# Kernel tuning notes

Measured on AMD Instinct MI355X. Metric: run time of the kernel, lower is better.

## Reference

```python
import jax, jax.numpy as jnp
import numpy as np

B, S, E = 2, 1024, 1024
H, DH = 16, 64           # num_heads, key_dim = E // H
MAXLEN = 2048            # config.max_sequence_length -> table size 2*MAXLEN-1


def setup_inputs() -> dict:
    key = jax.random.key(0)
    ks = jax.random.split(key, 13)
    sc = 1.0 / np.sqrt(E)
    return {
        "query": jax.random.normal(ks[0], (B, S, E), jnp.float32),
        "key": jax.random.normal(ks[1], (B, S, E), jnp.float32),
        "value": jax.random.normal(ks[2], (B, S, E), jnp.float32),
        "Wq": jax.random.normal(ks[3], (E, E), jnp.float32) * sc,
        "bq": jnp.zeros((E,), jnp.float32),
        "Wk": jax.random.normal(ks[4], (E, E), jnp.float32) * sc,
        "bk": jnp.zeros((E,), jnp.float32),
        "Wv": jax.random.normal(ks[5], (E, E), jnp.float32) * sc,
        "bv": jnp.zeros((E,), jnp.float32),
        "Wo": jax.random.normal(ks[6], (E, E), jnp.float32) * sc,
        "bo": jnp.zeros((E,), jnp.float32),
        "rel_pos_emb": jax.random.normal(ks[7], (2 * MAXLEN - 1, DH), jnp.float32) * 0.02,
        "rel_pos_bias": jnp.zeros((2 * MAXLEN - 1,), jnp.float32),
    }


def _split_heads(x):
    # [B, S, E] -> [B, H, S, DH]
    return x.reshape(B, S, H, DH).transpose(0, 2, 1, 3)


def _relative_shift(x):
    # x: [B, H, S, S]; pad one zero column on the left of the last dim,
    # reshape to [B, H, S+1, S], drop the first row -> [B, H, S, S]
    x = jnp.pad(x, ((0, 0), (0, 0), (0, 0), (1, 0)))
    x = x.reshape(B, H, S + 1, S)
    return x[:, :, 1:, :]


def reference(query, key, value, Wq, bq, Wk, bk, Wv, bv, Wo, bo,
              rel_pos_emb, rel_pos_bias):
    q = _split_heads(query @ Wq + bq) / jnp.sqrt(jnp.float32(DH))  # [B,H,S,DH]
    k = _split_heads(key @ Wk + bk)                                 # [B,H,S,DH]
    v = _split_heads(value @ Wv + bv)                               # [B,H,S,DH]

    scores = jnp.einsum("bhid,bhjd->bhij", q, k)  # [B,H,S,S]

    # relative position term (gather + skew, as in the original call())
    pos_ids = jnp.arange(S)[:, None] - jnp.arange(S)[None, :] + (MAXLEN - 1)  # [S,S]
    rpe = rel_pos_emb[pos_ids]    # [S, S, DH]
    rpb = rel_pos_bias[pos_ids]   # [S, S]
    rel = jnp.einsum("bhid,ijd->bhij", q, rpe)  # [B,H,S,S]
    rel = _relative_shift(rel)
    scores = scores + rel + rpb   # rpb broadcasts over [B,H]

    weights = jax.nn.softmax(scores, axis=-1)
    out = jnp.einsum("bhij,bhjd->bhid", weights, v)  # [B,H,S,DH]
    out = out.transpose(0, 2, 1, 3).reshape(B, S, E)
    return out @ Wo + bo
```

## Files before the change

### kernel.cpp

```cpp
#include <hip/hip_runtime.h>

typedef unsigned short u16;
typedef __bf16 bf16_t;
typedef bf16_t bf16x8 __attribute__((ext_vector_type(8)));
typedef u16 u16x8 __attribute__((ext_vector_type(8)));
typedef float f32x4 __attribute__((ext_vector_type(4)));

#define DEVI __device__ __forceinline__


DEVI u16 f2bf(float f) {
    unsigned u = __builtin_bit_cast(unsigned, f);
    u = (u + 0x7FFFu + ((u >> 16) & 1u)) >> 16;
    return (u16)u;
}
DEVI float bf2f(u16 b) {
    unsigned u = ((unsigned)b) << 16;
    return __builtin_bit_cast(float, u);
}
DEVI f32x4 mfma16(u16x8 a, u16x8 b, f32x4 c) {
    return __builtin_amdgcn_mfma_f32_16x16x32_bf16(
        __builtin_bit_cast(bf16x8, a), __builtin_bit_cast(bf16x8, b), c, 0, 0, 0);
}
DEVI void gl2lds(const u16* g, u16* l) {
    __builtin_amdgcn_global_load_lds(
        (__attribute__((address_space(1))) void*)g,
        (__attribute__((address_space(3))) void*)l, 16, 0, 0);
}

__global__ __launch_bounds__(256) void cvt_kernel(
    const float* __restrict__ q, const float* __restrict__ k, const float* __restrict__ v,
    const float* __restrict__ emb,
    u16* __restrict__ xq, u16* __restrict__ xk, u16* __restrict__ xv, u16* __restrict__ embb)
{
    const long NQ = 2097152;
    const long NE = 262080;
    long i4 = ((long)blockIdx.x * 256 + threadIdx.x) * 4;
    if (i4 < 3 * NQ) {
        int which = (int)(i4 >> 21);
        long off = i4 & (NQ - 1);
        const float* src = which == 0 ? q : (which == 1 ? k : v);
        u16* dst = which == 0 ? xq : (which == 1 ? xk : xv);
        float4 f = *(const float4*)(src + off);
        ushort4 o; o.x = f2bf(f.x); o.y = f2bf(f.y); o.z = f2bf(f.z); o.w = f2bf(f.w);
        *(ushort4*)(dst + off) = o;
    } else {
        long off = i4 - 3 * NQ;
        if (off < NE) {
            float4 f = *(const float4*)(emb + off);
            ushort4 o; o.x = f2bf(f.x); o.y = f2bf(f.y); o.z = f2bf(f.z); o.w = f2bf(f.w);
            *(ushort4*)(embb + off) = o;
        }
    }
}

__global__ __launch_bounds__(256) void wt_kernel(
    const float* __restrict__ w0, const float* __restrict__ w1,
    const float* __restrict__ w2, const float* __restrict__ w3,
    u16* __restrict__ t0, u16* __restrict__ t1, u16* __restrict__ t2, u16* __restrict__ t3)
{
    int z = blockIdx.z;
    const float* W = z == 0 ? w0 : (z == 1 ? w1 : (z == 2 ? w2 : w3));
    u16* T = z == 0 ? t0 : (z == 1 ? t1 : (z == 2 ? t2 : t3));
    __shared__ float tile[64][65];
    int k0 = blockIdx.y * 64, n0 = blockIdx.x * 64;
    int tx = threadIdx.x, ty = threadIdx.y;
    for (int r = ty; r < 64; r += 4)
        tile[r][tx] = W[(long)(k0 + r) * 1024 + n0 + tx];
    __syncthreads();
    for (int r = ty; r < 64; r += 4)
        T[(long)(n0 + r) * 1024 + k0 + tx] = f2bf(tile[tx][r]);
}

template<int MT>
__global__ __launch_bounds__(256) void gemm_kernel(
    const u16* __restrict__ A0, const u16* __restrict__ A1, const u16* __restrict__ A2,
    const u16* __restrict__ W0, const u16* __restrict__ W1, const u16* __restrict__ W2,
    const float* __restrict__ bias0, const float* __restrict__ bias1, const float* __restrict__ bias2,
    u16* __restrict__ o0, u16* __restrict__ o1, u16* __restrict__ o2,
    float* __restrict__ ofp, int mode_base)
{
    int z = blockIdx.z;
    int mode = mode_base + z;
    const u16* A = z == 0 ? A0 : (z == 1 ? A1 : A2);
    const u16* W = z == 0 ? W0 : (z == 1 ? W1 : W2);
    const float* bias = z == 0 ? bias0 : (z == 1 ? bias1 : bias2);
    u16* ob = z == 0 ? o0 : (z == 1 ? o1 : o2);

    constexpr int MROWS = MT * 32;
    __shared__ u16 la[2 * MROWS * 32];
    __shared__ u16 lw[2 * 128 * 32];

    int lin = blockIdx.x + (blockIdx.y << 3);
    int xcd = lin & 7, idx = lin >> 3;
    int xt = (xcd & 1) * 4 + (idx & 3);
    int yt = (xcd >> 1) * 8 + (idx >> 2);
    int m0 = yt * MROWS, n0 = xt * 128;

    int t = threadIdx.x, lane = t & 63, wid = t >> 6;
    int l15 = lane & 15, quad = lane >> 4;
    int wm = (wid >> 1) * (MT * 16), wn = (wid & 1) * 64;
    int sr = lane >> 2, sp = lane & 3;

    f32x4 acc[MT][4] = {};

    auto stage = [&](int buf, int k0) {
#pragma unroll
        for (int q = 0; q < MT / 2; q++) {
            int r = wid * (MT * 8) + q * 16 + sr;
            int c = sp ^ ((r >> 1) & 3);
            gl2lds(A + (long)(m0 + r) * 1024 + k0 + c * 8,
                   la + buf * (MROWS * 32) + (wid * (MT * 8) + q * 16) * 32);
        }
#pragma unroll
        for (int q = 0; q < 2; q++) {
            int r = wid * 32 + q * 16 + sr;
            int c = sp ^ ((r >> 1) & 3);
            gl2lds(W + (long)(n0 + r) * 1024 + k0 + c * 8,
                   lw + buf * (128 * 32) + (wid * 32 + q * 16) * 32);
        }
    };

    stage(0, 0);
    __syncthreads();
    int cur = 0;
#pragma unroll 1
    for (int k0 = 0; k0 < 1024; k0 += 32) {
        if (k0 < 992) stage(cur ^ 1, k0 + 32);
        const u16* lab = la + cur * (MROWS * 32);
        const u16* lwb = lw + cur * (128 * 32);
        u16x8 af[MT], bfr[4];
#pragma unroll
        for (int mt = 0; mt < MT; mt++) {
            int r = wm + mt * 16 + l15;
            af[mt] = *(const u16x8*)&lab[r * 32 + ((quad ^ ((r >> 1) & 3)) * 8)];
        }
#pragma unroll
        for (int nt = 0; nt < 4; nt++) {
            int r = wn + nt * 16 + l15;
            bfr[nt] = *(const u16x8*)&lwb[r * 32 + ((quad ^ ((r >> 1) & 3)) * 8)];
        }
#pragma unroll
        for (int mt = 0; mt < MT; mt++)
#pragma unroll
            for (int nt = 0; nt < 4; nt++)
                acc[mt][nt] = mfma16(af[mt], bfr[nt], acc[mt][nt]);
        __syncthreads();
        cur ^= 1;
    }

#pragma unroll
    for (int mt = 0; mt < MT; mt++)
#pragma unroll
        for (int nt = 0; nt < 4; nt++)
#pragma unroll
            for (int reg = 0; reg < 4; reg++) {
                int gm = m0 + wm + mt * 16 + quad * 4 + reg;
                int gn = n0 + wn + nt * 16 + l15;
                float val = acc[mt][nt][reg] + bias[gn];
                if (mode == 0) {
                    val *= 0.125f;
                    long o = ((long)((gm >> 10) * 16 + (gn >> 6)) << 16) + ((gm & 1023) << 6) + (gn & 63);
                    ob[o] = f2bf(val);
                } else if (mode == 1) {
                    long o = ((long)((gm >> 10) * 16 + (gn >> 6)) << 16) + ((gm & 1023) << 6) + (gn & 63);
                    ob[o] = f2bf(val);
                } else if (mode == 2) {
                    long o = ((long)((gm >> 10) * 16 + (gn >> 6)) << 16) + ((long)(gn & 63) << 10) + (gm & 1023);
                    ob[o] = f2bf(val);
                } else {
                    ofp[(long)gm * 1024 + gn] = val;
                }
            }
}

__global__ __launch_bounds__(256) void gc_kernel(
    const u16* __restrict__ qb, const u16* __restrict__ embb,
    const float* __restrict__ rpb, u16* __restrict__ Bskew)
{
    int u0 = blockIdx.x * 32;
    int i0 = u0 & 1023;
    int t = threadIdx.x, lane = t & 63, wid = t >> 6;
    int l15 = lane & 15, quad = lane >> 4;

    __shared__ float lds_rpb[2048];
    for (int j = t; j < 1024; j += 256) {
        lds_rpb[j] = rpb[j + 2047];
        lds_rpb[1024 + j] = rpb[j + 1022];
    }
    __syncthreads();

    u16x8 aq[2][2];
#pragma unroll
    for (int rg = 0; rg < 2; rg++) {
        long qoff = (long)(u0 + rg * 16 + l15) * 64 + quad * 8;
        aq[rg][0] = *(const u16x8*)&qb[qoff];
        aq[rg][1] = *(const u16x8*)&qb[qoff + 32];
    }

    u16x8 nb0, nb1;
    {
        long ebase = (long)(1024 + i0 + wid * 16 + l15) * 64 + quad * 8;
        nb0 = *(const u16x8*)&embb[ebase];
        nb1 = *(const u16x8*)&embb[ebase + 32];
    }

    for (int tt = wid; tt < 66; tt += 4) {
        u16x8 b0 = nb0, b1 = nb1;
        if (tt + 4 < 66) {
            long ebase = (long)(1024 + i0 + (tt + 4) * 16 + l15) * 64 + quad * 8;
            nb0 = *(const u16x8*)&embb[ebase];
            nb1 = *(const u16x8*)&embb[ebase + 32];
        }
        int w0 = tt * 16;
#pragma unroll
        for (int rg = 0; rg < 2; rg++) {
            f32x4 c = {};
            c = mfma16(aq[rg][0], b0, c);
            c = mfma16(aq[rg][1], b1, c);
#pragma unroll
            for (int reg = 0; reg < 4; reg++) {
                int row = rg * 16 + quad * 4 + reg;
                int cc = w0 + l15 - row;
                if ((unsigned)cc <= 1023u) {
                    int i = i0 + row;
                    float rb = lds_rpb[cc + ((cc <= i) ? 0 : 1024)];
                    Bskew[((long)(u0 + row) << 10) + cc] = f2bf(c[reg] + rb);
                }
            }
        }
    }
}

__global__ __launch_bounds__(256, 4) void flash_kernel(
    const u16* __restrict__ qb, const u16* __restrict__ kb, const u16* __restrict__ vT,
    const u16* __restrict__ Bskew, const float* __restrict__ rpb,
    float* __restrict__ Po, float* __restrict__ Pm, float* __restrict__ Pl)
{
    int itile = blockIdx.x;
    int bh = blockIdx.y;
    int js = blockIdx.z;
    int t = threadIdx.x, lane = t & 63, wid = t >> 6;
    int l15 = lane & 15, quad = lane >> 4;
    int i0w = itile * 64 + wid * 16;

    __shared__ u16 lds_k[64 * 64];
    __shared__ u16 lds_v[64 * 64];
    __shared__ u16 lds_p[4][16][72];

    int sr8 = lane >> 3, sp8 = lane & 7;

    float rpb2046 = rpb[2046];

    u16x8 aq[2];
    {
        long qoff = ((long)(bh * 1024) + i0w + l15) * 64 + quad * 8;
        aq[0] = *(const u16x8*)&qb[qoff];
        aq[1] = *(const u16x8*)&qb[qoff + 32];
    }
    float m_r[4], l_r[4];
    f32x4 o_acc[4] = {};
#pragma unroll
    for (int r = 0; r < 4; r++) { m_r[r] = -1e30f; l_r[r] = 0.f; }

    const u16* kbase = kb + (long)bh * 65536;
    const u16* vbase = vT + (long)bh * 65536;
    const u16* bbase = Bskew + ((long)bh << 20);

    for (int jt = 0; jt < 8; jt++) {
        int j0 = js * 512 + jt * 64;
        __syncthreads();
#pragma unroll
        for (int q = 0; q < 2; q++) {
            int r = wid * 16 + q * 8 + sr8;
            int c = sp8 ^ (r & 7);
            gl2lds(kbase + (long)(j0 + r) * 64 + c * 8, lds_k + (wid * 16 + q * 8) * 64);
            gl2lds(vbase + (long)r * 1024 + j0 + c * 8, lds_v + (wid * 16 + q * 8) * 64);
        }
        __syncthreads();

        f32x4 s_acc[4];
#pragma unroll
        for (int nt = 0; nt < 4; nt++) {
            int r = nt * 16 + l15;
            u16x8 b0 = *(const u16x8*)&lds_k[r * 64 + ((quad ^ (r & 7)) * 8)];
            u16x8 b1 = *(const u16x8*)&lds_k[r * 64 + (((quad + 4) ^ (r & 7)) * 8)];
            f32x4 c = {};
            c = mfma16(aq[0], b0, c);
            c = mfma16(aq[1], b1, c);
            s_acc[nt] = c;
        }

#pragma unroll
        for (int nt = 0; nt < 4; nt++) {
            int jn0 = j0 + nt * 16;
            int jj = jn0 + l15;
            if (jn0 + 15 <= i0w) {
#pragma unroll
                for (int reg = 0; reg < 4; reg++) {
                    int ii = i0w + quad * 4 + reg;
                    s_acc[nt][reg] += bf2f(bbase[((long)ii << 10) + (ii - jj)]);
                }
            } else if (jn0 >= i0w + 17) {
#pragma unroll
                for (int reg = 0; reg < 4; reg++) {
                    int ii = i0w + quad * 4 + reg;
                    s_acc[nt][reg] += bf2f(bbase[((long)(ii + 1) << 10) + (ii + 1025 - jj)]);
                }
            } else {
#pragma unroll
                for (int reg = 0; reg < 4; reg++) {
                    int ii = i0w + quad * 4 + reg;
                    float a;
                    if (jj <= ii)          a = bf2f(bbase[((long)ii << 10) + (ii - jj)]);
                    else if (jj == ii + 1) a = rpb2046;
                    else                   a = bf2f(bbase[((long)(ii + 1) << 10) + (ii + 1025 - jj)]);
                    s_acc[nt][reg] += a;
                }
            }
        }

#pragma unroll
        for (int reg = 0; reg < 4; reg++) {
            float mx = fmaxf(fmaxf(s_acc[0][reg], s_acc[1][reg]), fmaxf(s_acc[2][reg], s_acc[3][reg]));
            for (int off = 1; off < 16; off <<= 1) mx = fmaxf(mx, __shfl_xor(mx, off, 64));
            float mnew = fmaxf(m_r[reg], mx);
            float alpha = __expf(m_r[reg] - mnew);
            float rs = 0.f;
#pragma unroll
            for (int nt = 0; nt < 4; nt++) {
                float p = __expf(s_acc[nt][reg] - mnew);
                s_acc[nt][reg] = p;
                rs += p;
            }
            for (int off = 1; off < 16; off <<= 1) rs += __shfl_xor(rs, off, 64);
            l_r[reg] = l_r[reg] * alpha + rs;
            m_r[reg] = mnew;
#pragma unroll
            for (int dt = 0; dt < 4; dt++) o_acc[dt][reg] *= alpha;
        }

#pragma unroll
        for (int nt = 0; nt < 4; nt++)
#pragma unroll
            for (int reg = 0; reg < 4; reg++)
                lds_p[wid][quad * 4 + reg][nt * 16 + l15] = f2bf(s_acc[nt][reg]);

        u16x8 pf0 = *(const u16x8*)&lds_p[wid][l15][quad * 8];
        u16x8 pf1 = *(const u16x8*)&lds_p[wid][l15][quad * 8 + 32];
#pragma unroll
        for (int dt = 0; dt < 4; dt++) {
            int r = dt * 16 + l15;
            u16x8 v0 = *(const u16x8*)&lds_v[r * 64 + ((quad ^ (r & 7)) * 8)];
            u16x8 v1 = *(const u16x8*)&lds_v[r * 64 + (((quad + 4) ^ (r & 7)) * 8)];
            o_acc[dt] = mfma16(pf0, v0, o_acc[dt]);
            o_acc[dt] = mfma16(pf1, v1, o_acc[dt]);
        }
    }

    int blk = (js * 32 + bh) * 16 + itile;
    float* PoB = Po + (long)blk * 4096;
#pragma unroll
    for (int dt = 0; dt < 4; dt++)
#pragma unroll
        for (int reg = 0; reg < 4; reg++) {
            int rr = wid * 16 + quad * 4 + reg;
            PoB[rr * 64 + dt * 16 + l15] = o_acc[dt][reg];
        }
    if (l15 == 0) {
#pragma unroll
        for (int reg = 0; reg < 4; reg++) {
            int rr = wid * 16 + quad * 4 + reg;
            Pm[blk * 64 + rr] = m_r[reg];
            Pl[blk * 64 + rr] = l_r[reg];
        }
    }
}

__global__ __launch_bounds__(256) void combine_kernel(
    const float* __restrict__ Po, const float* __restrict__ Pm, const float* __restrict__ Pl,
    u16* __restrict__ attn)
{
    int itile = blockIdx.x, bh = blockIdx.y;
    int t = threadIdx.x;
    int c = t & 63, rg = t >> 6;
    int blk0 = bh * 16 + itile;
    int blk1 = (32 + bh) * 16 + itile;
    int b = bh >> 4, h = bh & 15;
    for (int rr = rg; rr < 64; rr += 4) {
        float m0 = Pm[blk0 * 64 + rr], m1 = Pm[blk1 * 64 + rr];
        float ms = fmaxf(m0, m1);
        float e0 = __expf(m0 - ms), e1 = __expf(m1 - ms);
        float l = Pl[blk0 * 64 + rr] * e0 + Pl[blk1 * 64 + rr] * e1;
        float o = Po[(long)blk0 * 4096 + rr * 64 + c] * e0
                + Po[(long)blk1 * 4096 + rr * 64 + c] * e1;
        int ii = itile * 64 + rr;
        attn[((long)(b * 1024 + ii)) * 1024 + h * 64 + c] = f2bf(o / l);
    }
}

extern "C" void kernel_launch(void* const* d_in, const int* in_sizes, int n_in,
                              void* d_out, int out_size, void* d_ws, size_t ws_size,
                              hipStream_t stream)
{
    const float* query = (const float*)d_in[0];
    const float* key_  = (const float*)d_in[1];
    const float* value = (const float*)d_in[2];
    const float* Wq = (const float*)d_in[3];
    const float* bq = (const float*)d_in[4];
    const float* Wk = (const float*)d_in[5];
    const float* bk = (const float*)d_in[6];
    const float* Wv = (const float*)d_in[7];
    const float* bv = (const float*)d_in[8];
    const float* Wo = (const float*)d_in[9];
    const float* bo = (const float*)d_in[10];
    const float* emb = (const float*)d_in[11];
    const float* rpb = (const float*)d_in[12];

    char* ws = (char*)d_ws;
    u16* xq   = (u16*)(ws + 0);
    u16* xk   = (u16*)(ws + 4194304);
    u16* xv   = (u16*)(ws + 8388608);
    u16* WqT  = (u16*)(ws + 12582912);
    u16* WkT  = (u16*)(ws + 14680064);
    u16* WvT  = (u16*)(ws + 16777216);
    u16* embb = (u16*)(ws + 18874368);
    u16* WoT  = (u16*)(ws + 19922944);
    u16* qb   = (u16*)(ws + 22020096);
    u16* kb   = (u16*)(ws + 26214400);
    u16* vT   = (u16*)(ws + 30408704);
    u16* Bskew= (u16*)(ws + 34603008);
    float* Po = (float*)(ws + 0);
    float* Pm = (float*)(ws + 16777216);
    float* Pl = (float*)(ws + 17039360);
    u16* attn = (u16*)(ws + 22020096);

    cvt_kernel<<<6400, 256, 0, stream>>>(query, key_, value, emb, xq, xk, xv, embb);
    wt_kernel<<<dim3(16, 16, 4), dim3(64, 4), 0, stream>>>(Wq, Wk, Wv, Wo, WqT, WkT, WvT, WoT);
    gemm_kernel<2><<<dim3(8, 32, 3), 256, 0, stream>>>(xq, xk, xv, WqT, WkT, WvT,
                                                       bq, bk, bv, qb, kb, vT, nullptr, 0);
    gc_kernel<<<1024, 256, 0, stream>>>(qb, embb, rpb, Bskew);
    flash_kernel<<<dim3(16, 32, 2), 256, 0, stream>>>(qb, kb, vT, Bskew, rpb, Po, Pm, Pl);
    combine_kernel<<<dim3(16, 32), 256, 0, stream>>>(Po, Pm, Pl, attn);
    gemm_kernel<2><<<dim3(8, 32, 1), 256, 0, stream>>>(attn, nullptr, nullptr, WoT, nullptr, nullptr,
                                                       bo, nullptr, nullptr,
                                                       nullptr, nullptr, nullptr, (float*)d_out, 3);
}
```

Measured before the change: 240.1 us.

## Double-buffer K/V tiles and prefetch skewed bias one iteration ahead

Switches the flash attention kernel to double-buffered LDS for the K and V tiles, so the next tile is issued while the current one is computed, and drops one barrier per iteration. It also prefetches the skewed relative-position bias values for the next tile into registers, taking scattered global-load latency off the critical path. In exchange, LDS use doubles and register pressure rises (16 extra prefetch registers), and occupancy is lowered from 4 to 3 blocks per SIMD in launch bounds. The diagonal tile's special case now loads a dummy element and overrides it with rpb[2046].

```diff
diff --git a/kernel.cpp b/kernel.cpp
--- a/kernel.cpp
+++ b/kernel.cpp
@@ -232,7 +232,7 @@
     }
 }
 
-__global__ __launch_bounds__(256, 4) void flash_kernel(
+__global__ __launch_bounds__(256, 3) void flash_kernel(
     const u16* __restrict__ qb, const u16* __restrict__ kb, const u16* __restrict__ vT,
     const u16* __restrict__ Bskew, const float* __restrict__ rpb,
     float* __restrict__ Po, float* __restrict__ Pm, float* __restrict__ Pl)
@@ -244,8 +244,8 @@
     int l15 = lane & 15, quad = lane >> 4;
     int i0w = itile * 64 + wid * 16;
 
-    __shared__ u16 lds_k[64 * 64];
-    __shared__ u16 lds_v[64 * 64];
+    __shared__ u16 lds_k[2][64 * 64];
+    __shared__ u16 lds_v[2][64 * 64];
     __shared__ u16 lds_p[4][16][72];
 
     int sr8 = lane >> 3, sp8 = lane & 7;
@@ -267,24 +267,64 @@
     const u16* vbase = vT + (long)bh * 65536;
     const u16* bbase = Bskew + ((long)bh << 20);
 
-    for (int jt = 0; jt < 8; jt++) {
-        int j0 = js * 512 + jt * 64;
-        __syncthreads();
+    auto stage = [&](int buf, int j0) {
 #pragma unroll
         for (int q = 0; q < 2; q++) {
             int r = wid * 16 + q * 8 + sr8;
             int c = sp8 ^ (r & 7);
-            gl2lds(kbase + (long)(j0 + r) * 64 + c * 8, lds_k + (wid * 16 + q * 8) * 64);
-            gl2lds(vbase + (long)r * 1024 + j0 + c * 8, lds_v + (wid * 16 + q * 8) * 64);
-        }
-        __syncthreads();
+            gl2lds(kbase + (long)(j0 + r) * 64 + c * 8, &lds_k[buf][(wid * 16 + q * 8) * 64]);
+            gl2lds(vbase + (long)r * 1024 + j0 + c * 8, &lds_v[buf][(wid * 16 + q * 8) * 64]);
+        }
+    };
+    auto ldb = [&](int j0, unsigned short* b) {
+#pragma unroll
+        for (int nt = 0; nt < 4; nt++) {
+            int jn0 = j0 + nt * 16;
+            int jj = jn0 + l15;
+            if (jn0 + 15 <= i0w) {
+#pragma unroll
+                for (int reg = 0; reg < 4; reg++) {
+                    int ii = i0w + quad * 4 + reg;
+                    b[nt * 4 + reg] = bbase[((long)ii << 10) + (ii - jj)];
+                }
+            } else if (jn0 >= i0w + 17) {
+#pragma unroll
+                for (int reg = 0; reg < 4; reg++) {
+                    int ii = i0w + quad * 4 + reg;
+                    b[nt * 4 + reg] = bbase[((long)(ii + 1) << 10) + (ii + 1025 - jj)];
+                }
+            } else {
+#pragma unroll
+                for (int reg = 0; reg < 4; reg++) {
+                    int ii = i0w + quad * 4 + reg;
+                    long off = (jj <= ii) ? (((long)ii << 10) + (ii - jj))
+                             : ((jj == ii + 1) ? ((long)ii << 10)
+                                               : (((long)(ii + 1) << 10) + (ii + 1025 - jj)));
+                    b[nt * 4 + reg] = bbase[off];
+                }
+            }
+        }
+    };
+
+    unsigned short bcur[16], bnxt[16];
+    stage(0, js * 512);
+    ldb(js * 512, bcur);
+    __syncthreads();
+
+    int cur = 0;
+    for (int jt = 0; jt < 8; jt++) {
+        int j0 = js * 512 + jt * 64;
+        if (jt < 7) {
+            stage(cur ^ 1, j0 + 64);
+            ldb(j0 + 64, bnxt);
+        }
 
         f32x4 s_acc[4];
 #pragma unroll
         for (int nt = 0; nt < 4; nt++) {
             int r = nt * 16 + l15;
-            u16x8 b0 = *(const u16x8*)&lds_k[r * 64 + ((quad ^ (r & 7)) * 8)];
-            u16x8 b1 = *(const u16x8*)&lds_k[r * 64 + (((quad + 4) ^ (r & 7)) * 8)];
+            u16x8 b0 = *(const u16x8*)&lds_k[cur][r * 64 + ((quad ^ (r & 7)) * 8)];
+            u16x8 b1 = *(const u16x8*)&lds_k[cur][r * 64 + (((quad + 4) ^ (r & 7)) * 8)];
             f32x4 c = {};
             c = mfma16(aq[0], b0, c);
             c = mfma16(aq[1], b1, c);
@@ -295,28 +335,13 @@
         for (int nt = 0; nt < 4; nt++) {
             int jn0 = j0 + nt * 16;
             int jj = jn0 + l15;
-            if (jn0 + 15 <= i0w) {
-#pragma unroll
-                for (int reg = 0; reg < 4; reg++) {
-                    int ii = i0w + quad * 4 + reg;
-                    s_acc[nt][reg] += bf2f(bbase[((long)ii << 10) + (ii - jj)]);
-                }
-            } else if (jn0 >= i0w + 17) {
-#pragma unroll
-                for (int reg = 0; reg < 4; reg++) {
-                    int ii = i0w + quad * 4 + reg;
-                    s_acc[nt][reg] += bf2f(bbase[((long)(ii + 1) << 10) + (ii + 1025 - jj)]);
-                }
-            } else {
-#pragma unroll
-                for (int reg = 0; reg < 4; reg++) {
-                    int ii = i0w + quad * 4 + reg;
-                    float a;
-                    if (jj <= ii)          a = bf2f(bbase[((long)ii << 10) + (ii - jj)]);
-                    else if (jj == ii + 1) a = rpb2046;
-                    else                   a = bf2f(bbase[((long)(ii + 1) << 10) + (ii + 1025 - jj)]);
-                    s_acc[nt][reg] += a;
-                }
+            bool mixed = (jn0 + 15 > i0w) && (jn0 < i0w + 17);
+#pragma unroll
+            for (int reg = 0; reg < 4; reg++) {
+                int ii = i0w + quad * 4 + reg;
+                float a = bf2f(bcur[nt * 4 + reg]);
+                if (mixed && jj == ii + 1) a = rpb2046;
+                s_acc[nt][reg] += a;
             }
         }
 
@@ -351,10 +376,17 @@
 #pragma unroll
         for (int dt = 0; dt < 4; dt++) {
             int r = dt * 16 + l15;
-            u16x8 v0 = *(const u16x8*)&lds_v[r * 64 + ((quad ^ (r & 7)) * 8)];
-            u16x8 v1 = *(const u16x8*)&lds_v[r * 64 + (((quad + 4) ^ (r & 7)) * 8)];
+            u16x8 v0 = *(const u16x8*)&lds_v[cur][r * 64 + ((quad ^ (r & 7)) * 8)];
+            u16x8 v1 = *(const u16x8*)&lds_v[cur][r * 64 + (((quad + 4) ^ (r & 7)) * 8)];
             o_acc[dt] = mfma16(pf0, v0, o_acc[dt]);
             o_acc[dt] = mfma16(pf1, v1, o_acc[dt]);
+        }
+
+        __syncthreads();
+        cur ^= 1;
+        if (jt < 7) {
+#pragma unroll
+            for (int q = 0; q < 16; q++) bcur[q] = bnxt[q];
         }
     }
 
```

New measurement: 263.5 us. +9.7%, slower.

## Double-buffer K/V tiles in flash kernel and generalize GEMM tile mapping

Applied to the files above, without the earlier changes.

The flash attention kernel now double-buffers the K and V LDS tiles, prefetching the next 64-column tile while computing the current one, and drops one of the two barriers per iteration. The P scratch buffer is changed from a padded layout to an XOR-swizzled one to avoid bank conflicts. The GEMM kernel's tile-to-block mapping now uses gridDim.y instead of a hardcoded 8, and gains an MT==1 staging path so smaller M tiles can be used. Double buffering doubles the K/V LDS footprint, which may lower occupancy under launch_bounds(256,4).

```diff
diff --git a/kernel.cpp b/kernel.cpp
--- a/kernel.cpp
+++ b/kernel.cpp
@@ -93,8 +93,9 @@
 
     int lin = blockIdx.x + (blockIdx.y << 3);
     int xcd = lin & 7, idx = lin >> 3;
+    int gy4 = gridDim.y >> 2;
     int xt = (xcd & 1) * 4 + (idx & 3);
-    int yt = (xcd >> 1) * 8 + (idx >> 2);
+    int yt = (xcd >> 1) * gy4 + (idx >> 2);
     int m0 = yt * MROWS, n0 = xt * 128;
 
     int t = threadIdx.x, lane = t & 63, wid = t >> 6;
@@ -105,12 +106,21 @@
     f32x4 acc[MT][4] = {};
 
     auto stage = [&](int buf, int k0) {
-#pragma unroll
-        for (int q = 0; q < MT / 2; q++) {
-            int r = wid * (MT * 8) + q * 16 + sr;
-            int c = sp ^ ((r >> 1) & 3);
-            gl2lds(A + (long)(m0 + r) * 1024 + k0 + c * 8,
-                   la + buf * (MROWS * 32) + (wid * (MT * 8) + q * 16) * 32);
+        if constexpr (MT == 1) {
+            if (wid < 2) {
+                int r = wid * 16 + sr;
+                int c = sp ^ ((r >> 1) & 3);
+                gl2lds(A + (long)(m0 + r) * 1024 + k0 + c * 8,
+                       la + buf * (MROWS * 32) + (wid * 16) * 32);
+            }
+        } else {
+#pragma unroll
+            for (int q = 0; q < MT / 2; q++) {
+                int r = wid * (MT * 8) + q * 16 + sr;
+                int c = sp ^ ((r >> 1) & 3);
+                gl2lds(A + (long)(m0 + r) * 1024 + k0 + c * 8,
+                       la + buf * (MROWS * 32) + (wid * (MT * 8) + q * 16) * 32);
+            }
         }
 #pragma unroll
         for (int q = 0; q < 2; q++) {
@@ -244,9 +254,9 @@
     int l15 = lane & 15, quad = lane >> 4;
     int i0w = itile * 64 + wid * 16;
 
-    __shared__ u16 lds_k[64 * 64];
-    __shared__ u16 lds_v[64 * 64];
-    __shared__ u16 lds_p[4][16][72];
+    __shared__ u16 lds_k[2][64 * 64];
+    __shared__ u16 lds_v[2][64 * 64];
+    __shared__ u16 lds_p[4][1024];
 
     int sr8 = lane >> 3, sp8 = lane & 7;
 
@@ -267,24 +277,31 @@
     const u16* vbase = vT + (long)bh * 65536;
     const u16* bbase = Bskew + ((long)bh << 20);
 
-    for (int jt = 0; jt < 8; jt++) {
-        int j0 = js * 512 + jt * 64;
-        __syncthreads();
+    auto stage = [&](int buf, int j0) {
 #pragma unroll
         for (int q = 0; q < 2; q++) {
             int r = wid * 16 + q * 8 + sr8;
             int c = sp8 ^ (r & 7);
-            gl2lds(kbase + (long)(j0 + r) * 64 + c * 8, lds_k + (wid * 16 + q * 8) * 64);
-            gl2lds(vbase + (long)r * 1024 + j0 + c * 8, lds_v + (wid * 16 + q * 8) * 64);
-        }
-        __syncthreads();
+            gl2lds(kbase + (long)(j0 + r) * 64 + c * 8, &lds_k[buf][(wid * 16 + q * 8) * 64]);
+            gl2lds(vbase + (long)r * 1024 + j0 + c * 8, &lds_v[buf][(wid * 16 + q * 8) * 64]);
+        }
+    };
+
+    stage(0, js * 512);
+    __syncthreads();
+    int cur = 0;
+
+#pragma unroll 1
+    for (int jt = 0; jt < 8; jt++) {
+        int j0 = js * 512 + jt * 64;
+        if (jt < 7) stage(cur ^ 1, j0 + 64);
 
         f32x4 s_acc[4];
 #pragma unroll
         for (int nt = 0; nt < 4; nt++) {
             int r = nt * 16 + l15;
-            u16x8 b0 = *(const u16x8*)&lds_k[r * 64 + ((quad ^ (r & 7)) * 8)];
-            u16x8 b1 = *(const u16x8*)&lds_k[r * 64 + (((quad + 4) ^ (r & 7)) * 8)];
+            u16x8 b0 = *(const u16x8*)&lds_k[cur][r * 64 + ((quad ^ (r & 7)) * 8)];
+            u16x8 b1 = *(const u16x8*)&lds_k[cur][r * 64 + (((quad + 4) ^ (r & 7)) * 8)];
             f32x4 c = {};
             c = mfma16(aq[0], b0, c);
             c = mfma16(aq[1], b1, c);
@@ -343,19 +360,25 @@
 #pragma unroll
         for (int nt = 0; nt < 4; nt++)
 #pragma unroll
-            for (int reg = 0; reg < 4; reg++)
-                lds_p[wid][quad * 4 + reg][nt * 16 + l15] = f2bf(s_acc[nt][reg]);
-
-        u16x8 pf0 = *(const u16x8*)&lds_p[wid][l15][quad * 8];
-        u16x8 pf1 = *(const u16x8*)&lds_p[wid][l15][quad * 8 + 32];
+            for (int reg = 0; reg < 4; reg++) {
+                int row = quad * 4 + reg;
+                int pos = ((nt * 2 + (l15 >> 3)) ^ (row & 7)) * 8 + (l15 & 7);
+                lds_p[wid][row * 64 + pos] = f2bf(s_acc[nt][reg]);
+            }
+
+        u16x8 pf0 = *(const u16x8*)&lds_p[wid][l15 * 64 + ((quad ^ (l15 & 7)) * 8)];
+        u16x8 pf1 = *(const u16x8*)&lds_p[wid][l15 * 64 + (((quad + 4) ^ (l15 & 7)) * 8)];
 #pragma unroll
         for (int dt = 0; dt < 4; dt++) {
             int r = dt * 16 + l15;
-            u16x8 v0 = *(const u16x8*)&lds_v[r * 64 + ((quad ^ (r & 7)) * 8)];
-            u16x8 v1 = *(const u16x8*)&lds_v[r * 64 + (((quad + 4) ^ (r & 7)) * 8)];
+            u16x8 v0 = *(const u16x8*)&lds_v[cur][r * 64 + ((quad ^ (r & 7)) * 8)];
+            u16x8 v1 = *(const u16x8*)&lds_v[cur][r * 64 + (((quad + 4) ^ (r & 7)) * 8)];
             o_acc[dt] = mfma16(pf0, v0, o_acc[dt]);
             o_acc[dt] = mfma16(pf1, v1, o_acc[dt]);
         }
+
+        __syncthreads();
+        cur ^= 1;
     }
 
     int blk = (js * 32 + bh) * 16 + itile;
```

New measurement: 245.0 us. 1.02x slower.
